# Optimization experiments

Measured on AMD Instinct MI355X. Metric: run time of the kernel, lower is better.

The kernel has to match this reference:

```python
import jax, jax.numpy as jnp
import numpy as np

B, S_IMG, S_TXT, P, D, HEADS, HD = 1, 2048, 512, 4, 3072, 24, 128


def rmsnorm(x, weight=None, eps=1e-6):
    var = jnp.mean(jnp.square(x), axis=-1, keepdims=True)
    y = x * jax.lax.rsqrt(var + eps)
    return y * weight if weight is not None else y


def apply_rope(x, cos, sin):
    # x: [B,H,S,Dh]; cos/sin: [S,Dh]; interleaved real/imag rotation (diffusers use_real_unbind_dim=-1)
    xr = x.reshape(*x.shape[:-1], -1, 2)
    rot = jnp.stack([-xr[..., 1], xr[..., 0]], axis=-1).reshape(x.shape)
    return x * cos[None, None] + rot * sin[None, None]


def sdpa(q, k, v):
    scores = jnp.einsum('bhqd,bhkd->bhqk', q, k) / jnp.sqrt(jnp.asarray(q.shape[-1], q.dtype))
    return jnp.einsum('bhqk,bhkd->bhqd', jax.nn.softmax(scores, axis=-1), v)


def heads_split(x):
    # [B,S,D] -> [B,H,S,Dh]
    return x.reshape(x.shape[0], x.shape[1], HEADS, HD).transpose(0, 2, 1, 3)


def heads_merge(x):
    # [B,H,S,Dh] -> [B,S,D]
    return x.transpose(0, 2, 1, 3).reshape(x.shape[0], x.shape[2], HEADS * HD)


def setup_inputs() -> dict:
    key = jax.random.key(0)
    ks = jax.random.split(key, 32)
    init = lambda k, shape: (jax.random.normal(k, shape, dtype=jnp.float32) * 0.02)
    inp = {
        'hidden_states': jax.random.normal(ks[0], (B, S_IMG, D), dtype=jnp.float32),
        'encoder_hidden_states': jax.random.normal(ks[1], (B, S_TXT, D), dtype=jnp.float32),
        'ip_encoder_hidden_states': jax.random.normal(ks[2], (B, P, D), dtype=jnp.float32),
        'layer_scale': jax.random.uniform(ks[3], (B,), dtype=jnp.float32),
        'Wq': init(ks[4], (D, D)), 'bq': jnp.zeros((D,), jnp.float32),
        'Wk': init(ks[5], (D, D)), 'bk': jnp.zeros((D,), jnp.float32),
        'Wv': init(ks[6], (D, D)), 'bv': jnp.zeros((D,), jnp.float32),
        'norm_q_w': jnp.ones((HD,), jnp.float32),
        'norm_k_w': jnp.ones((HD,), jnp.float32),
        'Waq': init(ks[7], (D, D)), 'baq': jnp.zeros((D,), jnp.float32),
        'Wak': init(ks[8], (D, D)), 'bak': jnp.zeros((D,), jnp.float32),
        'Wav': init(ks[9], (D, D)), 'bav': jnp.zeros((D,), jnp.float32),
        'norm_aq_w': jnp.ones((HD,), jnp.float32),
        'norm_ak_w': jnp.ones((HD,), jnp.float32),
        'Wk_ip': init(ks[10], (D, D)),
        'Wv_ip': init(ks[11], (D, D)),
        'Wo': init(ks[12], (D, D)), 'bo': jnp.zeros((D,), jnp.float32),
        'Wao': init(ks[13], (D, D)), 'bao': jnp.zeros((D,), jnp.float32),
    }
    # rotary cos/sin over the joint (text+image) sequence, interleaved freqs per diffusers FLUX
    pos = jnp.arange(S_TXT + S_IMG, dtype=jnp.float32)
    inv_freq = 1.0 / (10000.0 ** (jnp.arange(0, HD, 2, dtype=jnp.float32) / HD))
    angles = pos[:, None] * inv_freq[None, :]            # [S, HD/2]
    angles = jnp.repeat(angles, 2, axis=-1)              # [S, HD]
    inp['cos'] = jnp.cos(angles)
    inp['sin'] = jnp.sin(angles)
    return inp


IP_SCALE = 1.0  # self.scale


def reference(hidden_states, encoder_hidden_states, ip_encoder_hidden_states, cos, sin,
              layer_scale, Wq, bq, Wk, bk, Wv, bv, norm_q_w, norm_k_w,
              Waq, baq, Wak, bak, Wav, bav, norm_aq_w, norm_ak_w,
              Wk_ip, Wv_ip, Wo, bo, Wao, bao):
    # image-stream projections
    q = heads_split(hidden_states @ Wq.T + bq)
    k = heads_split(hidden_states @ Wk.T + bk)
    v = heads_split(hidden_states @ Wv.T + bv)
    q = rmsnorm(q, norm_q_w, 1e-6)
    k = rmsnorm(k, norm_k_w, 1e-6)

    # IP-adapter cross-attention (queries = image tokens, kv = IP tokens)
    ip_k = rmsnorm(heads_split(ip_encoder_hidden_states @ Wk_ip.T), None, 1e-5)
    ip_v = heads_split(ip_encoder_hidden_states @ Wv_ip.T)
    ip_out = heads_merge(sdpa(q, ip_k, ip_v))            # [B, S_img, D]

    # text (encoder) stream projections, prepended to joint sequence
    eq = rmsnorm(heads_split(encoder_hidden_states @ Waq.T + baq), norm_aq_w, 1e-6)
    ek = rmsnorm(heads_split(encoder_hidden_states @ Wak.T + bak), norm_ak_w, 1e-6)
    ev = heads_split(encoder_hidden_states @ Wav.T + bav)
    q = jnp.concatenate([eq, q], axis=2)
    k = jnp.concatenate([ek, k], axis=2)
    v = jnp.concatenate([ev, v], axis=2)

    q = apply_rope(q, cos, sin)
    k = apply_rope(k, cos, sin)

    out = heads_merge(sdpa(q, k, v))                     # [B, S_txt+S_img, D]
    n_txt = encoder_hidden_states.shape[1]
    enc_out, img_out = out[:, :n_txt], out[:, n_txt:]

    ls = layer_scale.reshape(-1, 1, 1)
    img_out = img_out + IP_SCALE * ls * ip_out
    img_out = img_out @ Wo.T + bo
    enc_out = enc_out @ Wao.T + bao
    return (img_out, enc_out)
```

## Files before the change

### kernel.cpp

```cpp
#include <hip/hip_runtime.h>

typedef _Float16 half_t;
typedef _Float16 half2v __attribute__((ext_vector_type(2)));
typedef _Float16 half4v __attribute__((ext_vector_type(4)));
typedef _Float16 half8v __attribute__((ext_vector_type(8)));
typedef float    float4v __attribute__((ext_vector_type(4)));
typedef short    short8v __attribute__((ext_vector_type(8)));

#define S_IMG 2048
#define S_TXT 512
#define S_TOT 2560
#define NH    24
#define HD    128
#define DM    3072
#define WSZC  9437184L
#define HSZC  6291456L
#define ESZC  1572864L

__device__ __forceinline__ void gload16(const void* g, void* l) {
  __builtin_amdgcn_global_load_lds(
      (const __attribute__((address_space(1))) unsigned int*)g,
      (__attribute__((address_space(3))) unsigned int*)l, 16, 0, 0);
}

__device__ __forceinline__ void cvt8span(const float* s, half_t* d, long i) {
  float4v v0 = *(const float4v*)(s + i);
  float4v v1 = *(const float4v*)(s + i + 4);
  half8v h;
  h[0] = (half_t)v0[0]; h[1] = (half_t)v0[1]; h[2] = (half_t)v0[2]; h[3] = (half_t)v0[3];
  h[4] = (half_t)v1[0]; h[5] = (half_t)v1[1]; h[6] = (half_t)v1[2]; h[7] = (half_t)v1[3];
  *(half8v*)(d + i) = h;
}

__global__ void cvt_act_kernel(const float* __restrict__ hs, const float* __restrict__ enc,
                               half_t* __restrict__ d) {
  const long TOT = HSZC + ESZC;
  long i = ((long)blockIdx.x * 256 + threadIdx.x) * 8;
  long stride = (long)gridDim.x * 256 * 8;
  for (; i < TOT; i += stride) {
    const float* s = i < HSZC ? hs + i : enc + (i - HSZC);
    half_t* dd = d + i;
    float4v v0 = *(const float4v*)(s);
    float4v v1 = *(const float4v*)(s + 4);
    half8v h;
    h[0] = (half_t)v0[0]; h[1] = (half_t)v0[1]; h[2] = (half_t)v0[2]; h[3] = (half_t)v0[3];
    h[4] = (half_t)v1[0]; h[5] = (half_t)v1[1]; h[6] = (half_t)v1[2]; h[7] = (half_t)v1[3];
    *(half8v*)dd = h;
  }
}

__global__ void cvt3_kernel(const float* __restrict__ s0, const float* __restrict__ s1,
                            const float* __restrict__ s2,
                            half_t* __restrict__ d0, half_t* __restrict__ d1,
                            half_t* __restrict__ d2, int n) {
  const float* s = blockIdx.y == 0 ? s0 : (blockIdx.y == 1 ? s1 : s2);
  half_t* d = blockIdx.y == 0 ? d0 : (blockIdx.y == 1 ? d1 : d2);
  long i = ((long)blockIdx.x * 256 + threadIdx.x) * 8;
  long stride = (long)gridDim.x * 256 * 8;
  for (; i < n; i += stride) cvt8span(s, d, i);
}

__global__ void cvt8_kernel(const float* w0, const float* w1, const float* w2,
                            const float* w3, const float* w4, const float* w5,
                            const float* hs, const float* enc,
                            half_t* __restrict__ W6, half_t* __restrict__ hs_h) {
  int y = blockIdx.y;
  const float* s;
  half_t* d;
  long n;
  if (y < 6) {
    s = y == 0 ? w0 : y == 1 ? w1 : y == 2 ? w2 : y == 3 ? w3 : y == 4 ? w4 : w5;
    d = W6 + (long)y * WSZC;
    n = WSZC;
  } else if (y == 6) { s = hs; d = hs_h; n = HSZC; }
  else               { s = enc; d = hs_h + HSZC; n = ESZC; }
  long i = ((long)blockIdx.x * 256 + threadIdx.x) * 8;
  long stride = (long)gridDim.x * 256 * 8;
  for (; i < n; i += stride) cvt8span(s, d, i);
}

template <typename OUT>
__device__ __forceinline__ void gemm_tile(half_t* As, half_t* Bs,
                                          const half_t* __restrict__ A,
                                          const half_t* __restrict__ Bt,
                                          const float* __restrict__ bias,
                                          OUT* __restrict__ C, int bm, int bn) {
  const int K = DM, N = DM;
  const int tid = threadIdx.x, wid = tid >> 6, l = tid & 63;
  const int wm = (wid >> 1) * 64, wn = (wid & 1) * 64;
  const int l15 = l & 15, l4 = l >> 4;
  float4v acc[4][4] = {};

  const int scol = ((l & 3) ^ ((l >> 3) & 3)) * 8;
  const half_t* ga = A + (long)(bm + wid * 32 + (l >> 2)) * K + scol;
  const half_t* gb = Bt + (long)(bn + wid * 32 + (l >> 2)) * K + scol;
  const long rowstep = 16l * K;

#define GSTAGE(T, SEL)                                                        \
  {                                                                           \
    char* a_d = (char*)As + (SEL) * 8192 + wid * 2048;                        \
    char* b_d = (char*)Bs + (SEL) * 8192 + wid * 2048;                        \
    int k0 = (T) * 32;                                                        \
    gload16(ga + k0, a_d);                                                    \
    gload16(ga + rowstep + k0, a_d + 1024);                                   \
    gload16(gb + k0, b_d);                                                    \
    gload16(gb + rowstep + k0, b_d + 1024);                                   \
  }

  GSTAGE(0, 0);

  const int NT = K / 32;
  const int cofs = (l4 * 16) ^ (((l15 >> 1) & 3) << 4);
  int sel = 0;
  for (int t = 0; t < NT; t++) {
    asm volatile("s_waitcnt vmcnt(0)" ::: "memory");
    __builtin_amdgcn_s_barrier();
    __builtin_amdgcn_sched_barrier(0);
    if (t + 1 < NT) GSTAGE(t + 1, sel ^ 1);
    __builtin_amdgcn_sched_barrier(0);
    const char* AsB = (const char*)As + sel * 8192;
    const char* BsB = (const char*)Bs + sel * 8192;
    half8v af[4], bf[4];
#pragma unroll
    for (int i = 0; i < 4; i++)
      af[i] = *(const half8v*)(AsB + (wm + i * 16 + l15) * 64 + cofs);
#pragma unroll
    for (int j = 0; j < 4; j++)
      bf[j] = *(const half8v*)(BsB + (wn + j * 16 + l15) * 64 + cofs);
    __builtin_amdgcn_s_setprio(1);
#pragma unroll
    for (int i = 0; i < 4; i++)
#pragma unroll
      for (int j = 0; j < 4; j++)
        acc[i][j] = __builtin_amdgcn_mfma_f32_16x16x32_f16(af[i], bf[j], acc[i][j], 0, 0, 0);
    __builtin_amdgcn_s_setprio(0);
    sel ^= 1;
  }
#undef GSTAGE
#pragma unroll
  for (int i = 0; i < 4; i++)
#pragma unroll
    for (int j = 0; j < 4; j++) {
      int row = bm + wm + i * 16 + l4 * 4;
      int col = bn + wn + j * 16 + l15;
      float bv = bias ? bias[col] : 0.0f;
#pragma unroll
      for (int r = 0; r < 4; r++) {
        float v = acc[i][j][r] + bv;
        C[(long)(row + r) * N + col] = (OUT)v;
      }
    }
}

__global__ __launch_bounds__(256) void gemm_qkv_kernel(
    const half_t* __restrict__ hs_h, const half_t* __restrict__ enc_h,
    const half_t* __restrict__ W6,
    const float* bq, const float* bk, const float* bv,
    const float* baq, const float* bak, const float* bav,
    half_t* q_raw, half_t* k_raw, half_t* v_raw,
    half_t* eq_r, half_t* ek_r, half_t* ev_r) {
  __shared__ half_t As[2 * 4096];
  __shared__ half_t Bs[2 * 4096];
  int b = blockIdx.x;
  int wg = (b & 7) * 180 + (b >> 3);
  const half_t* A;
  const half_t* Bt;
  const float* bias;
  half_t* C;
  int bm, bn;
  if (wg < 1152) {
    int col = wg / 16, row = wg % 16;
    int sel = col / 24;
    A = hs_h; bm = row * 128; bn = (col % 24) * 128;
    Bt = W6 + (long)sel * WSZC;
    bias = sel == 0 ? bq : (sel == 1 ? bk : bv);
    C = sel == 0 ? q_raw : (sel == 1 ? k_raw : v_raw);
  } else {
    int w2 = wg - 1152;
    int col = w2 / 4, row = w2 % 4;
    int sel = col / 24;
    A = enc_h; bm = row * 128; bn = (col % 24) * 128;
    Bt = W6 + (long)(3 + sel) * WSZC;
    bias = sel == 0 ? baq : (sel == 1 ? bak : bav);
    C = sel == 0 ? eq_r : (sel == 1 ? ek_r : ev_r);
  }
  gemm_tile<half_t>(As, Bs, A, Bt, bias, C, bm, bn);
}

template <int NROW>
__global__ __launch_bounds__(256) void gemm3_kernel(const half_t* __restrict__ A,
                                                    const half_t* __restrict__ W0,
                                                    const half_t* __restrict__ W1,
                                                    const half_t* __restrict__ W2,
                                                    const float* b0, const float* b1, const float* b2,
                                                    half_t* O0, half_t* O1, half_t* O2) {
  __shared__ half_t As[2 * 4096];
  __shared__ half_t Bs[2 * 4096];
  int b = blockIdx.x;
  int q = (72 * NROW) >> 3;
  int wg = (b & 7) * q + (b >> 3);
  int col = wg / NROW, row = wg % NROW;
  int sel = col / 24;
  const half_t* Bt = sel == 0 ? W0 : (sel == 1 ? W1 : W2);
  const float* bias = sel == 0 ? b0 : (sel == 1 ? b1 : b2);
  half_t* C = sel == 0 ? O0 : (sel == 1 ? O1 : O2);
  gemm_tile<half_t>(As, Bs, A, Bt, bias, C, row * 128, (col % 24) * 128);
}

__global__ __launch_bounds__(256) void gemm_out_kernel(const half_t* __restrict__ ocomb,
                                                       const half_t* __restrict__ Wo_h,
                                                       const half_t* __restrict__ Wao_h,
                                                       const float* bo, const float* bao,
                                                       float* out_img, float* out_enc) {
  __shared__ half_t As[2 * 4096];
  __shared__ half_t Bs[2 * 4096];
  int b = blockIdx.x;
  int wg = (b & 7) * 60 + (b >> 3);
  int col = wg / 20, r = wg % 20;
  bool enc = r >= 16;
  const half_t* A = enc ? ocomb : ocomb + (long)S_TXT * DM;
  int bm = (enc ? (r - 16) : r) * 128;
  gemm_tile<float>(As, Bs, A, enc ? Wao_h : Wo_h, enc ? bao : bo,
                   enc ? out_enc : out_img, bm, col * 128);
}

__global__ __launch_bounds__(256) void ip_proj_kernel(const float* __restrict__ x,
                                                      const float* __restrict__ Wk_ip,
                                                      const float* __restrict__ Wv_ip,
                                                      float* __restrict__ outk,
                                                      float* __restrict__ outv) {
  const float* W = blockIdx.y ? Wv_ip : Wk_ip;
  float* out = blockIdx.y ? outv : outk;
  int n = blockIdx.x * 4 + (threadIdx.x >> 6);
  int l = threadIdx.x & 63;
  const float* wr = W + (long)n * DM;
  float acc[4] = {0.f, 0.f, 0.f, 0.f};
  for (int k = l * 4; k < DM; k += 256) {
    float4v wv = *(const float4v*)(wr + k);
#pragma unroll
    for (int p = 0; p < 4; p++) {
      float4v xv = *(const float4v*)(x + p * DM + k);
      acc[p] += wv[0] * xv[0] + wv[1] * xv[1] + wv[2] * xv[2] + wv[3] * xv[3];
    }
  }
#pragma unroll
  for (int off = 32; off; off >>= 1)
#pragma unroll
    for (int p = 0; p < 4; p++) acc[p] += __shfl_xor(acc[p], off, 64);
  if (l == 0)
#pragma unroll
    for (int p = 0; p < 4; p++) out[p * DM + n] = acc[p];
}

__global__ void ip_norm_kernel(const float* __restrict__ kr, const float* __restrict__ vr,
                               half_t* __restrict__ kh, half_t* __restrict__ vh) {
  int t = blockIdx.x;
  int l = threadIdx.x;
  int d = l * 2;
  if (t < 96) {
    int base = (t / 24) * DM + (t % 24) * HD;
    float x0 = kr[base + d], x1 = kr[base + d + 1];
    float ss = x0 * x0 + x1 * x1;
#pragma unroll
    for (int off = 32; off; off >>= 1) ss += __shfl_xor(ss, off, 64);
    float r = rsqrtf(ss * (1.0f / HD) + 1e-5f);
    kh[base + d] = (half_t)(x0 * r);
    kh[base + d + 1] = (half_t)(x1 * r);
  } else {
    int t2 = t - 96;
    int base = (t2 / 24) * DM + (t2 % 24) * HD;
    vh[base + d] = (half_t)vr[base + d];
    vh[base + d + 1] = (half_t)vr[base + d + 1];
  }
}

__global__ __launch_bounds__(256) void prep_vtrans_kernel(
    const half_t* __restrict__ qraw, const half_t* __restrict__ kraw,
    const half_t* __restrict__ eq, const half_t* __restrict__ ek,
    const half_t* __restrict__ ev, const half_t* __restrict__ vraw,
    const float* __restrict__ nqw, const float* __restrict__ nkw,
    const float* __restrict__ naqw, const float* __restrict__ nakw,
    const float* __restrict__ cosb, const float* __restrict__ sinb,
    half_t* __restrict__ qcat, half_t* __restrict__ kcat, half_t* __restrict__ qnr,
    half_t* __restrict__ vcatT) {
  __shared__ half_t T[64][136];
  if (blockIdx.x < 15360) {
    int task = blockIdx.x * 4 + (threadIdx.x >> 6);
    int l = threadIdx.x & 63;
    int s = task / NH, h = task - (task / NH) * NH;
    int d = l * 2;
    const half_t *qs, *ks;
    const float *wq, *wk;
    if (s < S_TXT) {
      long base = (long)s * DM + h * HD;
      qs = eq + base; ks = ek + base;
      wq = naqw; wk = nakw;
    } else {
      long base = (long)(s - S_TXT) * DM + h * HD;
      qs = qraw + base; ks = kraw + base;
      wq = nqw; wk = nkw;
    }
    half2v qv = *(const half2v*)(qs + d);
    half2v kv = *(const half2v*)(ks + d);
    float q0 = (float)qv[0], q1 = (float)qv[1];
    float k0 = (float)kv[0], k1 = (float)kv[1];
    float ssq = q0 * q0 + q1 * q1;
    float ssk = k0 * k0 + k1 * k1;
#pragma unroll
    for (int off = 32; off; off >>= 1) {
      ssq += __shfl_xor(ssq, off, 64);
      ssk += __shfl_xor(ssk, off, 64);
    }
    float rq = rsqrtf(ssq * (1.0f / HD) + 1e-6f);
    float rk = rsqrtf(ssk * (1.0f / HD) + 1e-6f);
    float qn0 = q0 * rq * wq[d], qn1 = q1 * rq * wq[d + 1];
    float kn0 = k0 * rk * wk[d], kn1 = k1 * rk * wk[d + 1];
    if (s >= S_TXT) {
      half2v o; o[0] = (half_t)qn0; o[1] = (half_t)qn1;
      *(half2v*)(qnr + ((long)h * S_IMG + (s - S_TXT)) * HD + d) = o;
    }
    float c0 = cosb[s * HD + d], c1 = cosb[s * HD + d + 1];
    float s0 = sinb[s * HD + d], s1 = sinb[s * HD + d + 1];
    float qo0 = qn0 * c0 - qn1 * s0, qo1 = qn1 * c1 + qn0 * s1;
    float ko0 = kn0 * c0 - kn1 * s0, ko1 = kn1 * c1 + kn0 * s1;
    long ci = ((long)h * S_TOT + s) * HD + d;
    half2v oq; oq[0] = (half_t)qo0; oq[1] = (half_t)qo1;
    half2v ok; ok[0] = (half_t)ko0; ok[1] = (half_t)ko1;
    *(half2v*)(qcat + ci) = oq;
    *(half2v*)(kcat + ci) = ok;
  } else {
    int b2 = blockIdx.x - 15360;
    int h = b2 / 40, sb = (b2 % 40) * 64;
    int t = threadIdx.x;
#pragma unroll
    for (int i = 0; i < 4; i++) {
      int c = t + i * 256;
      int row = c >> 4, col = (c & 15) * 8;
      int s = sb + row;
      const half_t* src = (s < S_TXT) ? ev + (long)s * DM + h * HD + col
                                      : vraw + (long)(s - S_TXT) * DM + h * HD + col;
      *(half8v*)&T[row][col] = *(const half8v*)src;
    }
    __syncthreads();
#pragma unroll
    for (int i = 0; i < 4; i++) {
      int c = t + i * 256;
      int d = c >> 3, sc = (c & 7) * 8;
      half8v v;
#pragma unroll
      for (int j = 0; j < 8; j++) v[j] = T[sc + j][d];
      int base = (sc & 32) | ((sc & 8) << 1) | ((sc & 16) >> 2);
      half_t* dst = vcatT + ((long)h * HD + d) * S_TOT + sb;
      half4v q0; q0[0] = v[0]; q0[1] = v[1]; q0[2] = v[2]; q0[3] = v[3];
      half4v q1; q1[0] = v[4]; q1[1] = v[5]; q1[2] = v[6]; q1[3] = v[7];
      *(half4v*)(dst + base) = q0;
      *(half4v*)(dst + base + 8) = q1;
    }
  }
}

__global__ __launch_bounds__(256) void ip_attn_kernel(const half_t* __restrict__ qnr,
                                                      const half_t* __restrict__ kh,
                                                      const half_t* __restrict__ vh,
                                                      half_t* __restrict__ ipout) {
  int tid = threadIdx.x;
  int task = blockIdx.x * 16 + (tid >> 4);
  int l16 = tid & 15;
  int h = task >> 11;
  int s = task & 2047;
  int d = l16 * 8;
  half8v qv = *(const half8v*)(qnr + ((long)h * S_IMG + s) * HD + d);
  float sc[4];
#pragma unroll
  for (int p = 0; p < 4; p++) {
    half8v kv = *(const half8v*)(kh + p * DM + h * HD + d);
    float a = 0.f;
#pragma unroll
    for (int j = 0; j < 8; j++) a += (float)qv[j] * (float)kv[j];
    sc[p] = a;
  }
#pragma unroll
  for (int off = 8; off; off >>= 1)
#pragma unroll
    for (int p = 0; p < 4; p++) sc[p] += __shfl_xor(sc[p], off, 16);
  float m = fmaxf(fmaxf(sc[0], sc[1]), fmaxf(sc[2], sc[3]));
  float e[4], sum = 0.f;
#pragma unroll
  for (int p = 0; p < 4; p++) { e[p] = __expf((sc[p] - m) * 0.088388347648318447f); sum += e[p]; }
  float inv = 1.0f / sum;
  float o[8] = {};
#pragma unroll
  for (int p = 0; p < 4; p++) {
    half8v vv = *(const half8v*)(vh + p * DM + h * HD + d);
#pragma unroll
    for (int j = 0; j < 8; j++) o[j] += e[p] * (float)vv[j];
  }
  half8v ov;
#pragma unroll
  for (int j = 0; j < 8; j++) ov[j] = (half_t)(o[j] * inv);
  *(half8v*)(ipout + (long)s * DM + h * HD + d) = ov;
}

__global__ __launch_bounds__(256, 2) void flash_kernel(const half_t* __restrict__ qcat,
                                                       const half_t* __restrict__ kcat,
                                                       const half_t* __restrict__ vcatT,
                                                       const half_t* __restrict__ ipout,
                                                       const float* __restrict__ lsp,
                                                       half_t* __restrict__ ocomb,
                                                       const float* __restrict__ WoF,
                                                       const float* __restrict__ WaoF,
                                                       half_t* __restrict__ w0d,
                                                       half_t* __restrict__ w1d) {
  __shared__ half_t Ks[2 * 64 * 128];
  __shared__ half_t Vs[2 * 128 * 64];
  if (blockIdx.x >= 480) {
    int cb = blockIdx.x - 480;
    long i = ((long)cb * 256 + threadIdx.x) * 8;
    long stride = (long)(gridDim.x - 480) * 256 * 8;
    for (; i < 2 * WSZC; i += stride) {
      if (i < WSZC) cvt8span(WoF, w0d, i);
      else          cvt8span(WaoF, w1d, i - WSZC);
    }
    return;
  }
  int b = blockIdx.x;
  int wg = (b & 7) * 60 + (b >> 3);
  const int h = wg / 20, qb = wg % 20;
  const int tid = threadIdx.x, wid = tid >> 6, l = tid & 63;
  const int l15 = l & 15, l4 = l >> 4;
  const float CEXP = 0.12754137969983614f;

  half8v qf[2][4];
#pragma unroll
  for (int t = 0; t < 2; t++) {
    int qrow = qb * 128 + wid * 32 + t * 16 + l15;
    const half_t* qp = qcat + ((long)h * S_TOT + qrow) * HD;
#pragma unroll
    for (int kk = 0; kk < 4; kk++) qf[t][kk] = *(const half8v*)(qp + kk * 32 + l4 * 8);
  }
  float4v o[2][8] = {};
  float lsum[2] = {0.f, 0.f};
  const float ls = lsp[0];

  const char* kb = (const char*)(kcat + (long)h * S_TOT * HD);
  const char* vb = (const char*)(vcatT + (long)h * HD * S_TOT);
  int kof[4];
  long vof[4];
#pragma unroll
  for (int c = 0; c < 4; c++) {
    int L = c * 4096 + tid * 16;
    kof[c] = L ^ (((L >> 8) & 7) << 4);
    int vrow = L >> 7;
    vof[c] = (long)vrow * (S_TOT * 2) + ((L & 127) ^ ((vrow & 7) << 4));
  }

#define STAGE(KT, SEL)                                                        \
  {                                                                           \
    char* kd = (char*)Ks + (SEL) * 16384 + wid * 1024;                        \
    char* vd = (char*)Vs + (SEL) * 16384 + wid * 1024;                        \
    _Pragma("unroll") for (int c = 0; c < 4; c++) {                           \
      gload16(kb + (long)(KT) * 256 + kof[c], kd + c * 4096);                 \
      gload16(vb + vof[c] + (KT) * 2, vd + c * 4096);                         \
    }                                                                         \
  }

  STAGE(0, 0);

  const int NT = S_TOT / 64;
  int sel = 0;
  for (int it = 0; it < NT; it++) {
    asm volatile("s_waitcnt vmcnt(0)" ::: "memory");
    __builtin_amdgcn_s_barrier();
    __builtin_amdgcn_sched_barrier(0);
    if (it + 1 < NT) STAGE((it + 1) * 64, sel ^ 1);

    const char* KsB = (const char*)Ks + sel * 16384;
    const char* VsB = (const char*)Vs + sel * 16384;

    float4v s0[4] = {}, s1[4] = {};
    __builtin_amdgcn_s_setprio(1);
#pragma unroll
    for (int nb = 0; nb < 4; nb++) {
      int krow = nb * 16 + l15;
      int rb = krow << 8;
      int sw = (krow & 7) << 4;
#pragma unroll
      for (int kk = 0; kk < 4; kk++) {
        half8v kf = *(const half8v*)(KsB + rb + ((kk * 64 + l4 * 16) ^ sw));
        s0[nb] = __builtin_amdgcn_mfma_f32_16x16x32_f16(kf, qf[0][kk], s0[nb], 0, 0, 0);
        s1[nb] = __builtin_amdgcn_mfma_f32_16x16x32_f16(kf, qf[1][kk], s1[nb], 0, 0, 0);
      }
    }
    __builtin_amdgcn_s_setprio(0);
    half8v pa00, pa01, pa10, pa11;
    {
      float sum0 = 0.f, sum1 = 0.f;
      float e0[4][4], e1[4][4];
#pragma unroll
      for (int nb = 0; nb < 4; nb++)
#pragma unroll
        for (int r = 0; r < 4; r++) {
          float a = exp2f(s0[nb][r] * CEXP - 2.0f);
          float c = exp2f(s1[nb][r] * CEXP - 2.0f);
          e0[nb][r] = a; e1[nb][r] = c;
          sum0 += a; sum1 += c;
        }
      lsum[0] += sum0; lsum[1] += sum1;
#pragma unroll
      for (int r = 0; r < 4; r++) {
        pa00[r] = (half_t)e0[0][r]; pa00[r + 4] = (half_t)e0[1][r];
        pa01[r] = (half_t)e0[2][r]; pa01[r + 4] = (half_t)e0[3][r];
        pa10[r] = (half_t)e1[0][r]; pa10[r + 4] = (half_t)e1[1][r];
        pa11[r] = (half_t)e1[2][r]; pa11[r + 4] = (half_t)e1[3][r];
      }
    }
    __builtin_amdgcn_s_setprio(1);
#pragma unroll
    for (int cb = 0; cb < 8; cb++) {
      int row = cb * 16 + l15;
      int sw = (row & 7) << 4;
      half8v vf0 = *(const half8v*)(VsB + (row << 7) + ((l4 * 16) ^ sw));
      half8v vf1 = *(const half8v*)(VsB + (row << 7) + ((64 + l4 * 16) ^ sw));
      o[0][cb] = __builtin_amdgcn_mfma_f32_16x16x32_f16(pa00, vf0, o[0][cb], 0, 0, 0);
      o[0][cb] = __builtin_amdgcn_mfma_f32_16x16x32_f16(pa01, vf1, o[0][cb], 0, 0, 0);
      o[1][cb] = __builtin_amdgcn_mfma_f32_16x16x32_f16(pa10, vf0, o[1][cb], 0, 0, 0);
      o[1][cb] = __builtin_amdgcn_mfma_f32_16x16x32_f16(pa11, vf1, o[1][cb], 0, 0, 0);
    }
    __builtin_amdgcn_s_setprio(0);
    sel ^= 1;
  }
#undef STAGE
  float lreg[2];
#pragma unroll
  for (int t = 0; t < 2; t++) {
    float s = lsum[t];
    s += __shfl_xor(s, 16, 64);
    s += __shfl_xor(s, 32, 64);
    lreg[t] = s;
  }
#pragma unroll
  for (int t = 0; t < 2; t++) {
    float invq = 1.0f / lreg[t];
#pragma unroll
    for (int r = 0; r < 4; r++) {
      float inv = __shfl(invq, l4 * 4 + r, 64);
      int s = qb * 128 + wid * 32 + t * 16 + l4 * 4 + r;
#pragma unroll
      for (int cb = 0; cb < 8; cb++) {
        int col = h * HD + cb * 16 + l15;
        float val = o[t][cb][r] * inv;
        if (s >= S_TXT) val += ls * (float)ipout[(long)(s - S_TXT) * DM + col];
        ocomb[(long)s * DM + col] = (half_t)val;
      }
    }
  }
}

extern "C" void kernel_launch(void* const* d_in, const int* in_sizes, int n_in,
                              void* d_out, int out_size, void* d_ws, size_t ws_size,
                              hipStream_t stream) {
  (void)in_sizes; (void)n_in; (void)out_size;
  const float* hs    = (const float*)d_in[0];
  const float* enc   = (const float*)d_in[1];
  const float* ipenc = (const float*)d_in[2];
  const float* lsc   = (const float*)d_in[3];
  const float* Wq  = (const float*)d_in[4];  const float* bq  = (const float*)d_in[5];
  const float* Wk  = (const float*)d_in[6];  const float* bk  = (const float*)d_in[7];
  const float* Wv  = (const float*)d_in[8];  const float* bv  = (const float*)d_in[9];
  const float* nqw = (const float*)d_in[10]; const float* nkw = (const float*)d_in[11];
  const float* Waq = (const float*)d_in[12]; const float* baq = (const float*)d_in[13];
  const float* Wak = (const float*)d_in[14]; const float* bak = (const float*)d_in[15];
  const float* Wav = (const float*)d_in[16]; const float* bav = (const float*)d_in[17];
  const float* naqw= (const float*)d_in[18]; const float* nakw= (const float*)d_in[19];
  const float* Wkip= (const float*)d_in[20]; const float* Wvip= (const float*)d_in[21];
  const float* Wo  = (const float*)d_in[22]; const float* bo  = (const float*)d_in[23];
  const float* Wao = (const float*)d_in[24]; const float* bao = (const float*)d_in[25];
  const float* cosb= (const float*)d_in[26]; const float* sinb= (const float*)d_in[27];

  const size_t WSZ = WSZC;
  const size_t HSZ = HSZC;
  const size_t ESZ = ESZC;
  const size_t CSZ = (size_t)NH * S_TOT * HD;
  const size_t REST = HSZ + ESZ + 3 * HSZ + 3 * ESZ + 3 * CSZ;
  const bool big = ws_size >= (6 * WSZ + REST) * sizeof(half_t);
  const int NSLOT = big ? 6 : 3;

  half_t* base = (half_t*)d_ws;
  half_t* Wsl   = base;
  half_t* hs_h  = Wsl + NSLOT * WSZ;
  half_t* enc_h = hs_h + HSZ;
  half_t* qkvr  = enc_h + ESZ;
  half_t* eqkv  = qkvr + 3 * HSZ;
  half_t* qcat  = eqkv + 3 * ESZ;
  half_t* kcat  = qcat + CSZ;
  half_t* vcatT = kcat + CSZ;

  half_t* q_raw = qkvr;
  half_t* k_raw = qkvr + HSZ;
  half_t* v_raw = qkvr + 2 * HSZ;
  half_t* eq_r  = eqkv;
  half_t* ek_r  = eqkv + ESZ;
  half_t* ev_r  = eqkv + 2 * ESZ;
  half_t* qnr   = hs_h;
  half_t* ipout = qkvr;
  half_t* ocomb = qkvr + HSZ;
  float*  ipk_raw = (float*)enc_h;
  float*  ipv_raw = ipk_raw + 4 * DM;
  half_t* ipk_h  = enc_h + 16 * DM;
  half_t* ipv_h  = ipk_h + 4 * DM;

  if (big) {
    cvt8_kernel<<<dim3(1024, 8), 256, 0, stream>>>(Wq, Wk, Wv, Waq, Wak, Wav,
                                                   hs, enc, Wsl, hs_h);
    gemm_qkv_kernel<<<1440, 256, 0, stream>>>(hs_h, enc_h, Wsl,
                                              bq, bk, bv, baq, bak, bav,
                                              q_raw, k_raw, v_raw, eq_r, ek_r, ev_r);
  } else {
    cvt_act_kernel<<<2048, 256, 0, stream>>>(hs, enc, hs_h);
    cvt3_kernel<<<dim3(1024, 3), 256, 0, stream>>>(Wq, Wk, Wv, Wsl, Wsl + WSZ, Wsl + 2 * WSZ, (int)WSZ);
    gemm3_kernel<16><<<1152, 256, 0, stream>>>(hs_h, Wsl, Wsl + WSZ, Wsl + 2 * WSZ,
                                               bq, bk, bv, q_raw, k_raw, v_raw);
    cvt3_kernel<<<dim3(1024, 3), 256, 0, stream>>>(Waq, Wak, Wav, Wsl, Wsl + WSZ, Wsl + 2 * WSZ, (int)WSZ);
    gemm3_kernel<4><<<288, 256, 0, stream>>>(enc_h, Wsl, Wsl + WSZ, Wsl + 2 * WSZ,
                                             baq, bak, bav, eq_r, ek_r, ev_r);
  }

  ip_proj_kernel<<<dim3(768, 2), 256, 0, stream>>>(ipenc, Wkip, Wvip, ipk_raw, ipv_raw);
  ip_norm_kernel<<<192, 64, 0, stream>>>(ipk_raw, ipv_raw, ipk_h, ipv_h);

  prep_vtrans_kernel<<<16320, 256, 0, stream>>>(q_raw, k_raw, eq_r, ek_r, ev_r, v_raw,
                                                nqw, nkw, naqw, nakw, cosb, sinb,
                                                qcat, kcat, qnr, vcatT);

  ip_attn_kernel<<<(NH * S_IMG) / 16, 256, 0, stream>>>(qnr, ipk_h, ipv_h, ipout);

  if (big) {
    flash_kernel<<<480 + 512, 256, 0, stream>>>(qcat, kcat, vcatT, ipout, lsc, ocomb,
                                                Wo, Wao, Wsl, Wsl + WSZ);
  } else {
    flash_kernel<<<480, 256, 0, stream>>>(qcat, kcat, vcatT, ipout, lsc, ocomb,
                                          Wo, Wao, Wsl, Wsl + WSZ);
    cvt3_kernel<<<dim3(1024, 2), 256, 0, stream>>>(Wo, Wao, Wao, Wsl, Wsl + WSZ, Wsl + 2 * WSZ, (int)WSZ);
  }

  float* out_img = (float*)d_out;
  float* out_enc = (float*)d_out + (size_t)S_IMG * DM;
  gemm_out_kernel<<<480, 256, 0, stream>>>(ocomb, Wsl, Wsl + WSZ, bo, bao, out_img, out_enc);
}
```

Baseline: 500.2 us.

## Fuse fp32-to-fp16 weight conversion into QKV GEMM B-tile loads

The QKV projection GEMM now loads fp32 weights straight into shared memory and converts them to fp16 while building the MFMA fragments. This removes the separate conversion pass that wrote and reread six fp16 weight copies. It also drops the workspace-size branching, so only two weight slots are used and the flash kernel always converts Wo/Wao. In exchange the GEMM reads twice the weight bytes per tile, needs more LDS, and spends VALU on conversions inside the main loop, with each weight tile converted once per M tile.

```diff
diff --git a/kernel.cpp b/kernel.cpp
--- a/kernel.cpp
+++ b/kernel.cpp
@@ -39,44 +39,90 @@
   long stride = (long)gridDim.x * 256 * 8;
   for (; i < TOT; i += stride) {
     const float* s = i < HSZC ? hs + i : enc + (i - HSZC);
-    half_t* dd = d + i;
-    float4v v0 = *(const float4v*)(s);
-    float4v v1 = *(const float4v*)(s + 4);
-    half8v h;
-    h[0] = (half_t)v0[0]; h[1] = (half_t)v0[1]; h[2] = (half_t)v0[2]; h[3] = (half_t)v0[3];
-    h[4] = (half_t)v1[0]; h[5] = (half_t)v1[1]; h[6] = (half_t)v1[2]; h[7] = (half_t)v1[3];
-    *(half8v*)dd = h;
-  }
-}
-
-__global__ void cvt3_kernel(const float* __restrict__ s0, const float* __restrict__ s1,
-                            const float* __restrict__ s2,
-                            half_t* __restrict__ d0, half_t* __restrict__ d1,
-                            half_t* __restrict__ d2, int n) {
-  const float* s = blockIdx.y == 0 ? s0 : (blockIdx.y == 1 ? s1 : s2);
-  half_t* d = blockIdx.y == 0 ? d0 : (blockIdx.y == 1 ? d1 : d2);
-  long i = ((long)blockIdx.x * 256 + threadIdx.x) * 8;
-  long stride = (long)gridDim.x * 256 * 8;
-  for (; i < n; i += stride) cvt8span(s, d, i);
-}
-
-__global__ void cvt8_kernel(const float* w0, const float* w1, const float* w2,
-                            const float* w3, const float* w4, const float* w5,
-                            const float* hs, const float* enc,
-                            half_t* __restrict__ W6, half_t* __restrict__ hs_h) {
-  int y = blockIdx.y;
-  const float* s;
-  half_t* d;
-  long n;
-  if (y < 6) {
-    s = y == 0 ? w0 : y == 1 ? w1 : y == 2 ? w2 : y == 3 ? w3 : y == 4 ? w4 : w5;
-    d = W6 + (long)y * WSZC;
-    n = WSZC;
-  } else if (y == 6) { s = hs; d = hs_h; n = HSZC; }
-  else               { s = enc; d = hs_h + HSZC; n = ESZC; }
-  long i = ((long)blockIdx.x * 256 + threadIdx.x) * 8;
-  long stride = (long)gridDim.x * 256 * 8;
-  for (; i < n; i += stride) cvt8span(s, d, i);
+    cvt8span(s, d + i, 0);
+  }
+}
+
+__device__ __forceinline__ void gemm_tile_wf32(half_t* As, char* Bsc,
+                                               const half_t* __restrict__ A,
+                                               const float* __restrict__ Btf,
+                                               const float* __restrict__ bias,
+                                               half_t* __restrict__ C, int bm, int bn) {
+  const int K = DM, N = DM;
+  const int tid = threadIdx.x, wid = tid >> 6, l = tid & 63;
+  const int wm = (wid >> 1) * 64, wn = (wid & 1) * 64;
+  const int l15 = l & 15, l4 = l >> 4;
+  float4v acc[4][4] = {};
+
+  const int scolA = ((l & 3) ^ ((l >> 3) & 3)) * 8;
+  const half_t* ga = A + (long)(bm + wid * 32 + (l >> 2)) * K + scolA;
+  const long rowstepA = 16l * K;
+  const int sbyteB = ((tid & 7) * 16) ^ (((tid >> 3) & 7) << 4);
+  const float* gb = Btf + (long)(bn + (tid >> 3)) * K + (sbyteB >> 2);
+  const long rowstepB = 32l * K;
+
+#define GSTAGE(T, SEL)                                                        \
+  {                                                                           \
+    char* a_d = (char*)As + (SEL) * 8192 + wid * 2048;                        \
+    char* b_d = Bsc + (SEL) * 16384 + wid * 1024;                             \
+    int k0 = (T) * 32;                                                        \
+    gload16(ga + k0, a_d);                                                    \
+    gload16(ga + rowstepA + k0, a_d + 1024);                                  \
+    _Pragma("unroll") for (int c = 0; c < 4; c++)                             \
+      gload16(gb + c * rowstepB + k0, b_d + c * 4096);                        \
+  }
+
+  GSTAGE(0, 0);
+
+  const int NT = K / 32;
+  const int cofsA = (l4 * 16) ^ (((l15 >> 1) & 3) << 4);
+  int sel = 0;
+  for (int t = 0; t < NT; t++) {
+    asm volatile("s_waitcnt vmcnt(0)" ::: "memory");
+    __builtin_amdgcn_s_barrier();
+    __builtin_amdgcn_sched_barrier(0);
+    if (t + 1 < NT) GSTAGE(t + 1, sel ^ 1);
+    __builtin_amdgcn_sched_barrier(0);
+    const char* AsB = (const char*)As + sel * 8192;
+    const char* BsB = Bsc + sel * 16384;
+    half8v af[4], bf[4];
+#pragma unroll
+    for (int i = 0; i < 4; i++)
+      af[i] = *(const half8v*)(AsB + (wm + i * 16 + l15) * 64 + cofsA);
+#pragma unroll
+    for (int j = 0; j < 4; j++) {
+      int row = wn + j * 16 + l15;
+      int sw = (row & 7) << 4;
+      float4v b0 = *(const float4v*)(BsB + (row << 7) + ((l4 * 32) ^ sw));
+      float4v b1 = *(const float4v*)(BsB + (row << 7) + ((l4 * 32 + 16) ^ sw));
+      half8v hb;
+      hb[0] = (half_t)b0[0]; hb[1] = (half_t)b0[1]; hb[2] = (half_t)b0[2]; hb[3] = (half_t)b0[3];
+      hb[4] = (half_t)b1[0]; hb[5] = (half_t)b1[1]; hb[6] = (half_t)b1[2]; hb[7] = (half_t)b1[3];
+      bf[j] = hb;
+    }
+    __builtin_amdgcn_s_setprio(1);
+#pragma unroll
+    for (int i = 0; i < 4; i++)
+#pragma unroll
+      for (int j = 0; j < 4; j++)
+        acc[i][j] = __builtin_amdgcn_mfma_f32_16x16x32_f16(af[i], bf[j], acc[i][j], 0, 0, 0);
+    __builtin_amdgcn_s_setprio(0);
+    sel ^= 1;
+  }
+#undef GSTAGE
+#pragma unroll
+  for (int i = 0; i < 4; i++)
+#pragma unroll
+    for (int j = 0; j < 4; j++) {
+      int row = bm + wm + i * 16 + l4 * 4;
+      int col = bn + wn + j * 16 + l15;
+      float bv = bias[col];
+#pragma unroll
+      for (int r = 0; r < 4; r++) {
+        float v = acc[i][j][r] + bv;
+        C[(long)(row + r) * N + col] = (half_t)v;
+      }
+    }
 }
 
 template <typename OUT>
@@ -154,17 +200,18 @@
 
 __global__ __launch_bounds__(256) void gemm_qkv_kernel(
     const half_t* __restrict__ hs_h, const half_t* __restrict__ enc_h,
-    const half_t* __restrict__ W6,
+    const float* Wq, const float* Wk, const float* Wv,
+    const float* Waq, const float* Wak, const float* Wav,
     const float* bq, const float* bk, const float* bv,
     const float* baq, const float* bak, const float* bav,
     half_t* q_raw, half_t* k_raw, half_t* v_raw,
     half_t* eq_r, half_t* ek_r, half_t* ev_r) {
   __shared__ half_t As[2 * 4096];
-  __shared__ half_t Bs[2 * 4096];
+  __shared__ char   Bsc[2 * 16384];
   int b = blockIdx.x;
   int wg = (b & 7) * 180 + (b >> 3);
   const half_t* A;
-  const half_t* Bt;
+  const float* Bt;
   const float* bias;
   half_t* C;
   int bm, bn;
@@ -172,7 +219,7 @@
     int col = wg / 16, row = wg % 16;
     int sel = col / 24;
     A = hs_h; bm = row * 128; bn = (col % 24) * 128;
-    Bt = W6 + (long)sel * WSZC;
+    Bt = sel == 0 ? Wq : (sel == 1 ? Wk : Wv);
     bias = sel == 0 ? bq : (sel == 1 ? bk : bv);
     C = sel == 0 ? q_raw : (sel == 1 ? k_raw : v_raw);
   } else {
@@ -180,31 +227,11 @@
     int col = w2 / 4, row = w2 % 4;
     int sel = col / 24;
     A = enc_h; bm = row * 128; bn = (col % 24) * 128;
-    Bt = W6 + (long)(3 + sel) * WSZC;
+    Bt = sel == 0 ? Waq : (sel == 1 ? Wak : Wav);
     bias = sel == 0 ? baq : (sel == 1 ? bak : bav);
     C = sel == 0 ? eq_r : (sel == 1 ? ek_r : ev_r);
   }
-  gemm_tile<half_t>(As, Bs, A, Bt, bias, C, bm, bn);
-}
-
-template <int NROW>
-__global__ __launch_bounds__(256) void gemm3_kernel(const half_t* __restrict__ A,
-                                                    const half_t* __restrict__ W0,
-                                                    const half_t* __restrict__ W1,
-                                                    const half_t* __restrict__ W2,
-                                                    const float* b0, const float* b1, const float* b2,
-                                                    half_t* O0, half_t* O1, half_t* O2) {
-  __shared__ half_t As[2 * 4096];
-  __shared__ half_t Bs[2 * 4096];
-  int b = blockIdx.x;
-  int q = (72 * NROW) >> 3;
-  int wg = (b & 7) * q + (b >> 3);
-  int col = wg / NROW, row = wg % NROW;
-  int sel = col / 24;
-  const half_t* Bt = sel == 0 ? W0 : (sel == 1 ? W1 : W2);
-  const float* bias = sel == 0 ? b0 : (sel == 1 ? b1 : b2);
-  half_t* C = sel == 0 ? O0 : (sel == 1 ? O1 : O2);
-  gemm_tile<half_t>(As, Bs, A, Bt, bias, C, row * 128, (col % 24) * 128);
+  gemm_tile_wf32(As, Bsc, A, Bt, bias, C, bm, bn);
 }
 
 __global__ __launch_bounds__(256) void gemm_out_kernel(const half_t* __restrict__ ocomb,
@@ -559,7 +586,7 @@
 extern "C" void kernel_launch(void* const* d_in, const int* in_sizes, int n_in,
                               void* d_out, int out_size, void* d_ws, size_t ws_size,
                               hipStream_t stream) {
-  (void)in_sizes; (void)n_in; (void)out_size;
+  (void)in_sizes; (void)n_in; (void)out_size; (void)ws_size;
   const float* hs    = (const float*)d_in[0];
   const float* enc   = (const float*)d_in[1];
   const float* ipenc = (const float*)d_in[2];
@@ -581,13 +608,10 @@
   const size_t HSZ = HSZC;
   const size_t ESZ = ESZC;
   const size_t CSZ = (size_t)NH * S_TOT * HD;
-  const size_t REST = HSZ + ESZ + 3 * HSZ + 3 * ESZ + 3 * CSZ;
-  const bool big = ws_size >= (6 * WSZ + REST) * sizeof(half_t);
-  const int NSLOT = big ? 6 : 3;
 
   half_t* base = (half_t*)d_ws;
   half_t* Wsl   = base;
-  half_t* hs_h  = Wsl + NSLOT * WSZ;
+  half_t* hs_h  = Wsl + 2 * WSZ;
   half_t* enc_h = hs_h + HSZ;
   half_t* qkvr  = enc_h + ESZ;
   half_t* eqkv  = qkvr + 3 * HSZ;
@@ -609,21 +633,12 @@
   half_t* ipk_h  = enc_h + 16 * DM;
   half_t* ipv_h  = ipk_h + 4 * DM;
 
-  if (big) {
-    cvt8_kernel<<<dim3(1024, 8), 256, 0, stream>>>(Wq, Wk, Wv, Waq, Wak, Wav,
-                                                   hs, enc, Wsl, hs_h);
-    gemm_qkv_kernel<<<1440, 256, 0, stream>>>(hs_h, enc_h, Wsl,
-                                              bq, bk, bv, baq, bak, bav,
-                                              q_raw, k_raw, v_raw, eq_r, ek_r, ev_r);
-  } else {
-    cvt_act_kernel<<<2048, 256, 0, stream>>>(hs, enc, hs_h);
-    cvt3_kernel<<<dim3(1024, 3), 256, 0, stream>>>(Wq, Wk, Wv, Wsl, Wsl + WSZ, Wsl + 2 * WSZ, (int)WSZ);
-    gemm3_kernel<16><<<1152, 256, 0, stream>>>(hs_h, Wsl, Wsl + WSZ, Wsl + 2 * WSZ,
-                                               bq, bk, bv, q_raw, k_raw, v_raw);
-    cvt3_kernel<<<dim3(1024, 3), 256, 0, stream>>>(Waq, Wak, Wav, Wsl, Wsl + WSZ, Wsl + 2 * WSZ, (int)WSZ);
-    gemm3_kernel<4><<<288, 256, 0, stream>>>(enc_h, Wsl, Wsl + WSZ, Wsl + 2 * WSZ,
-                                             baq, bak, bav, eq_r, ek_r, ev_r);
-  }
+  cvt_act_kernel<<<2048, 256, 0, stream>>>(hs, enc, hs_h);
+
+  gemm_qkv_kernel<<<1440, 256, 0, stream>>>(hs_h, enc_h,
+                                            Wq, Wk, Wv, Waq, Wak, Wav,
+                                            bq, bk, bv, baq, bak, bav,
+                                            q_raw, k_raw, v_raw, eq_r, ek_r, ev_r);
 
   ip_proj_kernel<<<dim3(768, 2), 256, 0, stream>>>(ipenc, Wkip, Wvip, ipk_raw, ipv_raw);
   ip_norm_kernel<<<192, 64, 0, stream>>>(ipk_raw, ipv_raw, ipk_h, ipv_h);
@@ -634,14 +649,8 @@
 
   ip_attn_kernel<<<(NH * S_IMG) / 16, 256, 0, stream>>>(qnr, ipk_h, ipv_h, ipout);
 
-  if (big) {
-    flash_kernel<<<480 + 512, 256, 0, stream>>>(qcat, kcat, vcatT, ipout, lsc, ocomb,
-                                                Wo, Wao, Wsl, Wsl + WSZ);
-  } else {
-    flash_kernel<<<480, 256, 0, stream>>>(qcat, kcat, vcatT, ipout, lsc, ocomb,
-                                          Wo, Wao, Wsl, Wsl + WSZ);
-    cvt3_kernel<<<dim3(1024, 2), 256, 0, stream>>>(Wo, Wao, Wao, Wsl, Wsl + WSZ, Wsl + 2 * WSZ, (int)WSZ);
-  }
+  flash_kernel<<<480 + 512, 256, 0, stream>>>(qcat, kcat, vcatT, ipout, lsc, ocomb,
+                                              Wo, Wao, Wsl, Wsl + WSZ);
 
   float* out_img = (float*)d_out;
   float* out_enc = (float*)d_out + (size_t)S_IMG * DM;
```

Result: slower. 523.3 us (+4.6%).
